# Kernel tuning notes

Measured on AMD Instinct MI355X. Metric: run time of the kernel, lower is better.

## Reference

```python
import jax, jax.numpy as jnp
import numpy as np

N_NODES = 100000
N_EDGES = 1600000
N_FEAT = 128
HIDDEN = 128
N_GRAPHS = 1024


def setup_inputs() -> dict:
    key = jax.random.key(0)
    ks = jax.random.split(key, 9)
    x = jax.random.normal(ks[0], (N_NODES, N_FEAT), dtype=jnp.float32)
    edge_index = jax.random.randint(ks[1], (2, N_EDGES), 0, N_NODES, dtype=jnp.int64)
    batch = jnp.sort(jax.random.randint(ks[2], (N_NODES,), 0, N_GRAPHS, dtype=jnp.int64))
    W1 = jax.random.normal(ks[3], (N_FEAT, HIDDEN), dtype=jnp.float32) * (1.0 / np.sqrt(N_FEAT))
    b1 = jax.random.normal(ks[4], (HIDDEN,), dtype=jnp.float32) * 0.01
    W2 = jax.random.normal(ks[5], (HIDDEN, HIDDEN), dtype=jnp.float32) * (1.0 / np.sqrt(HIDDEN))
    b2 = jax.random.normal(ks[6], (HIDDEN,), dtype=jnp.float32) * 0.01
    Wl = jax.random.normal(ks[7], (HIDDEN, 2), dtype=jnp.float32) * (1.0 / np.sqrt(HIDDEN))
    bl = jax.random.normal(ks[8], (2,), dtype=jnp.float32) * 0.01
    return {"x": x, "edge_index": edge_index, "batch": batch,
            "W1": W1, "b1": b1, "W2": W2, "b2": b2, "Wl": Wl, "bl": bl}


def _gcn_norm(edge_index, num_nodes):
    # PyG GCNConv: add self-loops, then sym-normalize with in-degree (target col).
    loop = jnp.arange(num_nodes, dtype=edge_index.dtype)
    src = jnp.concatenate([edge_index[0], loop])  # [E+N]
    dst = jnp.concatenate([edge_index[1], loop])  # [E+N]
    deg = jax.ops.segment_sum(jnp.ones_like(dst, dtype=jnp.float32), dst,
                              num_segments=num_nodes)
    dinv = jnp.where(deg > 0, jax.lax.rsqrt(deg), 0.0)
    norm = dinv[src] * dinv[dst]  # [E+N]
    return src, dst, norm


def _gcn_conv(h, W, b, src, dst, norm, num_nodes):
    h = h @ W                                   # [N, out]
    msg = h[src] * norm[:, None]                # gather + scale, [E+N, out]
    agg = jax.ops.segment_sum(msg, dst, num_segments=num_nodes)  # scatter-add
    return agg + b


def reference(x, edge_index, batch, W1, b1, W2, b2, Wl, bl):
    n = x.shape[0]
    src, dst, norm = _gcn_norm(edge_index, n)
    h = jax.nn.relu(_gcn_conv(x, W1, b1, src, dst, norm, n))
    h = jax.nn.relu(_gcn_conv(h, W2, b2, src, dst, norm, n))
    # global_mean_pool over graph ids
    sums = jax.ops.segment_sum(h, batch, num_segments=N_GRAPHS)        # [G, H]
    counts = jax.ops.segment_sum(jnp.ones((n,), jnp.float32), batch,
                                 num_segments=N_GRAPHS)
    pooled = sums / jnp.maximum(counts, 1.0)[:, None]
    # F.dropout with training=False default in inference -> identity
    return pooled @ Wl + bl  # [G, 2]
```

## Files before the change

kernel.cpp:

```cpp
#include <hip/hip_runtime.h>
#include <hip/hip_bf16.h>

#define N_NODES 100000
#define N_EDGES 1600000
#define FEAT 128
#define N_GRAPHS 1024
#define NBUCK 391
#define CHUNK 4096
#define NTILES 1563
#define G1A 781
#define G1B 782

typedef short short8 __attribute__((ext_vector_type(8)));
typedef float float4v __attribute__((ext_vector_type(4)));

static __device__ inline unsigned short f2bf(float f) {
    __hip_bfloat16 b = __float2bfloat16(f);
    unsigned short r;
    __builtin_memcpy(&r, &b, 2);
    return r;
}
static __device__ inline float bf_lo(unsigned int v) { return __uint_as_float(v << 16); }
static __device__ inline float bf_hi(unsigned int v) { return __uint_as_float(v & 0xFFFF0000u); }

__global__ __launch_bounds__(256) void k_prep_hist(const float* __restrict__ W1,
                                                   const float* __restrict__ W2,
                                                   unsigned short* __restrict__ wp1,
                                                   unsigned short* __restrict__ wp2,
                                                   const int* __restrict__ dst,
                                                   int* __restrict__ bcount,
                                                   unsigned int* __restrict__ udummy,
                                                   unsigned int* __restrict__ u2dummy,
                                                   float* __restrict__ dinv) {
    int bid = blockIdx.x;
    if (bid < 128) {
        const float* W = (bid < 64) ? W1 : W2;
        unsigned short* wp = (bid < 64) ? wp1 : wp2;
        int t = (bid & 63) * 256 + threadIdx.x;
        int k = t >> 7, n = t & 127;
        float w = W[k * 128 + n];
        unsigned ub = __float_as_uint(w);
        unsigned short hi = (unsigned short)(ub >> 16);
        float hif = __uint_as_float(ub & 0xFFFF0000u);
        unsigned short lo = f2bf(w - hif);
        int sidx = n * 128 + ((k & 7) | (8 * (((k >> 3) ^ n) & 15)));
        wp[sidx] = hi;
        wp[16384 + sidx] = lo;
        if (bid == 0) {
            if (threadIdx.x < 64) udummy[threadIdx.x] = 0;
            else if (threadIdx.x < 128) u2dummy[threadIdx.x - 64] = 0;
            else if (threadIdx.x == 128) dinv[N_NODES] = 0.f;
        }
    } else {
        __shared__ int h[NBUCK];
        for (int i = threadIdx.x; i < NBUCK; i += 256) h[i] = 0;
        __syncthreads();
        int hb = bid - 128;
        for (int e = hb * 256 + threadIdx.x; e < N_EDGES; e += 256 * 256)
            atomicAdd(&h[dst[e] >> 8], 1);
        __syncthreads();
        for (int i = threadIdx.x; i < NBUCK; i += 256) {
            int c = h[i];
            if (c) atomicAdd(&bcount[i], c);
        }
    }
}

__global__ __launch_bounds__(512) void k_scan391(const int* __restrict__ in,
                                                 int* __restrict__ base,
                                                 int* __restrict__ cur,
                                                 int* __restrict__ tail) {
    int t = threadIdx.x;
    int v = (t < NBUCK) ? in[t] : 0;
    int lane = t & 63, wid = t >> 6;
    int s = v;
#pragma unroll
    for (int d = 1; d < 64; d <<= 1) { int n = __shfl_up(s, d); if (lane >= d) s += n; }
    __shared__ int ws[8];
    if (lane == 63) ws[wid] = s;
    __syncthreads();
    if (t < 8) {
        int x = ws[t];
#pragma unroll
        for (int d = 1; d < 8; d <<= 1) { int n = __shfl_up(x, d); if ((int)t >= d) x += n; }
        ws[t] = x;
    }
    __syncthreads();
    int excl = s - v + (wid ? ws[wid - 1] : 0);
    if (t < NBUCK) {
        base[t] = excl;
        cur[t] = excl;
    }
    if (t == 0) tail[0] = N_EDGES;
}

__device__ __forceinline__ void gemm_f32_body(int tile, const float* __restrict__ inp,
                                              const unsigned short* __restrict__ wp,
                                              unsigned short* __restrict__ u) {
    __shared__ unsigned short sW[32768];
    {
        float4* d4 = (float4*)sW;
        const float4* s4 = (const float4*)wp;
#pragma unroll
        for (int i = 0; i < 16; ++i) d4[threadIdx.x + 256 * i] = s4[threadIdx.x + 256 * i];
    }
    __syncthreads();
    const int t = threadIdx.x;
    const int wv = t >> 6, L = t & 63;
    const int m = L & 15, q = L >> 4;
    const int r0 = tile * 64 + wv * 16;
    int arow = r0 + m;
    if (arow >= N_NODES) arow = N_NODES - 1;
    const float4* ap = (const float4*)(inp + (size_t)arow * 128);
    float4v acc[8];
#pragma unroll
    for (int c = 0; c < 8; ++c) acc[c] = (float4v){0.f, 0.f, 0.f, 0.f};
#pragma unroll
    for (int k0 = 0; k0 < 128; k0 += 32) {
        float4 f0 = ap[(k0 >> 2) + 2 * q];
        float4 f1 = ap[(k0 >> 2) + 2 * q + 1];
        float fa[8] = {f0.x, f0.y, f0.z, f0.w, f1.x, f1.y, f1.z, f1.w};
        short8 ah, al;
#pragma unroll
        for (int j = 0; j < 8; ++j) {
            unsigned ub = __float_as_uint(fa[j]);
            ah[j] = (short)(ub >> 16);
            float hif = __uint_as_float(ub & 0xFFFF0000u);
            al[j] = (short)f2bf(fa[j] - hif);
        }
        const int b = (k0 >> 3) + q;
#pragma unroll
        for (int c = 0; c < 8; ++c) {
            int ng = c * 16 + m;
            int elem = ng * 128 + 8 * ((b ^ ng) & 15);
            short8 bh = *(const short8*)&sW[elem];
            short8 bl = *(const short8*)&sW[16384 + elem];
            acc[c] = __builtin_amdgcn_mfma_f32_16x16x32_bf16(ah, bh, acc[c], 0, 0, 0);
            acc[c] = __builtin_amdgcn_mfma_f32_16x16x32_bf16(al, bh, acc[c], 0, 0, 0);
            acc[c] = __builtin_amdgcn_mfma_f32_16x16x32_bf16(ah, bl, acc[c], 0, 0, 0);
        }
    }
#pragma unroll
    for (int r = 0; r < 4; ++r) {
        int row = r0 + 4 * q + r;
        if (row < N_NODES) {
            unsigned short* up = u + (size_t)row * 128 + m;
#pragma unroll
            for (int c = 0; c < 8; ++c) up[c * 16] = f2bf(acc[c][r]);
        }
    }
}

__global__ __launch_bounds__(256) void k_bucket_g1(const int* __restrict__ src,
                                                   const int* __restrict__ dst,
                                                   int* __restrict__ bcur,
                                                   unsigned int* __restrict__ pairs,
                                                   const float* __restrict__ x,
                                                   const unsigned short* __restrict__ wp1,
                                                   unsigned short* __restrict__ u) {
    if (blockIdx.x >= NBUCK) {
        gemm_f32_body(blockIdx.x - NBUCK, x, wp1, u);
        return;
    }
    __shared__ int cnt[NBUCK];
    __shared__ int basebuf[NBUCK];
    int t = threadIdx.x;
    int e0 = blockIdx.x * CHUNK;
    for (int i = t; i < NBUCK; i += 256) cnt[i] = 0;
    __syncthreads();
    unsigned pk[16]; int bk[16];
#pragma unroll
    for (int j = 0; j < 16; ++j) {
        int e = e0 + j * 256 + t;
        if (e < N_EDGES) {
            int s = src[e], d = dst[e];
            bk[j] = d >> 8;
            pk[j] = ((unsigned)s << 8) | (unsigned)(d & 255);
            atomicAdd(&cnt[bk[j]], 1);
        } else bk[j] = -1;
    }
    __syncthreads();
    for (int i = t; i < NBUCK; i += 256) {
        int c = cnt[i];
        basebuf[i] = c ? atomicAdd(&bcur[i], c) : 0;
        cnt[i] = 0;
    }
    __syncthreads();
#pragma unroll
    for (int j = 0; j < 16; ++j) {
        if (bk[j] >= 0) {
            int p = basebuf[bk[j]] + atomicAdd(&cnt[bk[j]], 1);
            pairs[p] = pk[j];
        }
    }
}

__global__ __launch_bounds__(256) void k_bfill_g1(const unsigned int* __restrict__ pairs,
                                                  const int* __restrict__ bbase,
                                                  const int* __restrict__ bcount,
                                                  float* __restrict__ dinv,
                                                  int* __restrict__ offs,
                                                  int* __restrict__ csr,
                                                  const float* __restrict__ x,
                                                  const unsigned short* __restrict__ wp1,
                                                  unsigned short* __restrict__ u) {
    if (blockIdx.x >= NBUCK) {
        gemm_f32_body(blockIdx.x - NBUCK + G1A, x, wp1, u);
        return;
    }
    __shared__ int degl[256];
    __shared__ int lcur[256];
    __shared__ int ws[4];
    int b = blockIdx.x, t = threadIdx.x;
    degl[t] = 0;
    __syncthreads();
    int s0 = bbase[b], n = bcount[b];
    for (int i = t; i < n; i += 256) atomicAdd(&degl[pairs[s0 + i] & 255u], 1);
    __syncthreads();
    int node = b * 256 + t;
    int dv = degl[t];
    if (node < N_NODES) dinv[node] = rsqrtf((float)(dv + 1));
    int lane = t & 63, wid = t >> 6;
    int s = dv;
#pragma unroll
    for (int d = 1; d < 64; d <<= 1) { int nn = __shfl_up(s, d); if (lane >= d) s += nn; }
    if (lane == 63) ws[wid] = s;
    __syncthreads();
    if (t < 4) {
        int xx = ws[t];
#pragma unroll
        for (int d = 1; d < 4; d <<= 1) { int nn = __shfl_up(xx, d); if ((int)t >= d) xx += nn; }
        ws[t] = xx;
    }
    __syncthreads();
    int excl = s - dv + (wid ? ws[wid - 1] : 0) + bbase[b];
    if (node < N_NODES) offs[node] = excl;
    lcur[t] = excl;
    __syncthreads();
    for (int i = t; i < n; i += 256) {
        unsigned pr = pairs[s0 + i];
        int p = atomicAdd(&lcur[pr & 255u], 1);
        csr[p] = (int)(pr >> 8);
    }
}

__global__ __launch_bounds__(512, 6) void k_agg1_g2(const unsigned int* __restrict__ u,
                                                    const int* __restrict__ offs,
                                                    const int* __restrict__ csr,
                                                    const float* __restrict__ dinv,
                                                    const float* __restrict__ bias,
                                                    const unsigned short* __restrict__ wp,
                                                    unsigned short* __restrict__ u2) {
    __shared__ float hS[32 * 128];
    const int w = threadIdx.x >> 6;
    const int lane = threadIdx.x & 63;
    const int base = blockIdx.x * 32;

    for (int n = 0; n < 4; ++n) {
        const int row = 4 * w + n;
        const int node = base + row;
        int p = __builtin_amdgcn_readfirstlane(offs[node]);
        int e = __builtin_amdgcn_readfirstlane(offs[node + 1]);
        float dsf = dinv[node];
        unsigned int self = u[(size_t)node * 64 + lane];
        float ax0 = dsf * bf_lo(self), ay0 = dsf * bf_hi(self);
        float ax1 = 0.f, ay1 = 0.f, ax2 = 0.f, ay2 = 0.f, ax3 = 0.f, ay3 = 0.f;
        float ax4 = 0.f, ay4 = 0.f, ax5 = 0.f, ay5 = 0.f, ax6 = 0.f, ay6 = 0.f;
        float ax7 = 0.f, ay7 = 0.f;
        for (; p < e; p += 8) {
            int c0 = csr[p + 0], c1 = csr[p + 1], c2 = csr[p + 2], c3 = csr[p + 3];
            int c4 = csr[p + 4], c5 = csr[p + 5], c6 = csr[p + 6], c7 = csr[p + 7];
            int i0 = c0;
            int i1 = (p + 1 < e) ? c1 : N_NODES;
            int i2 = (p + 2 < e) ? c2 : N_NODES;
            int i3 = (p + 3 < e) ? c3 : N_NODES;
            int i4 = (p + 4 < e) ? c4 : N_NODES;
            int i5 = (p + 5 < e) ? c5 : N_NODES;
            int i6 = (p + 6 < e) ? c6 : N_NODES;
            int i7 = (p + 7 < e) ? c7 : N_NODES;
            float d0 = dinv[i0], d1 = dinv[i1], d2 = dinv[i2], d3 = dinv[i3];
            float d4 = dinv[i4], d5 = dinv[i5], d6 = dinv[i6], d7 = dinv[i7];
            unsigned v0 = (u + (size_t)i0 * 64)[lane];
            unsigned v1 = (u + (size_t)i1 * 64)[lane];
            unsigned v2 = (u + (size_t)i2 * 64)[lane];
            unsigned v3 = (u + (size_t)i3 * 64)[lane];
            unsigned v4 = (u + (size_t)i4 * 64)[lane];
            unsigned v5 = (u + (size_t)i5 * 64)[lane];
            unsigned v6 = (u + (size_t)i6 * 64)[lane];
            unsigned v7 = (u + (size_t)i7 * 64)[lane];
            ax0 = fmaf(d0, bf_lo(v0), ax0); ay0 = fmaf(d0, bf_hi(v0), ay0);
            ax1 = fmaf(d1, bf_lo(v1), ax1); ay1 = fmaf(d1, bf_hi(v1), ay1);
            ax2 = fmaf(d2, bf_lo(v2), ax2); ay2 = fmaf(d2, bf_hi(v2), ay2);
            ax3 = fmaf(d3, bf_lo(v3), ax3); ay3 = fmaf(d3, bf_hi(v3), ay3);
            ax4 = fmaf(d4, bf_lo(v4), ax4); ay4 = fmaf(d4, bf_hi(v4), ay4);
            ax5 = fmaf(d5, bf_lo(v5), ax5); ay5 = fmaf(d5, bf_hi(v5), ay5);
            ax6 = fmaf(d6, bf_lo(v6), ax6); ay6 = fmaf(d6, bf_hi(v6), ay6);
            ax7 = fmaf(d7, bf_lo(v7), ax7); ay7 = fmaf(d7, bf_hi(v7), ay7);
        }
        float2 b = ((const float2*)bias)[lane];
        float sx = ((ax0 + ax1) + (ax2 + ax3)) + ((ax4 + ax5) + (ax6 + ax7));
        float sy = ((ay0 + ay1) + (ay2 + ay3)) + ((ay4 + ay5) + (ay6 + ay7));
        float r0 = fmaxf(dsf * sx + b.x, 0.f);
        float r1 = fmaxf(dsf * sy + b.y, 0.f);
        int g4 = (lane >> 1) ^ (row & 7);
        float2* hp = (float2*)&hS[row * 128 + g4 * 4 + (lane & 1) * 2];
        *hp = (float2){r0, r1};
    }

    const int m = lane & 15, q = lane >> 4;
    const int rt = w >> 2;
    const int cw = w & 3;
    const int arow = 16 * rt + m;
    const int ng0 = (2 * cw + 0) * 16 + m;
    const int ng1 = (2 * cw + 1) * 16 + m;
    short8 bh0, bl0, bh1, bl1;
    {
        int b = q;
        int e0 = ng0 * 128 + 8 * ((b ^ ng0) & 15);
        int e1 = ng1 * 128 + 8 * ((b ^ ng1) & 15);
        bh0 = *(const short8*)&wp[e0];
        bl0 = *(const short8*)&wp[16384 + e0];
        bh1 = *(const short8*)&wp[e1];
        bl1 = *(const short8*)&wp[16384 + e1];
    }
    __syncthreads();

    float4v acc0 = (float4v){0.f, 0.f, 0.f, 0.f};
    float4v acc1 = (float4v){0.f, 0.f, 0.f, 0.f};
#pragma unroll
    for (int ks = 0; ks < 4; ++ks) {
        short8 nh0, nl0, nh1, nl1;
        if (ks < 3) {
            int b = 4 * (ks + 1) + q;
            int e0 = ng0 * 128 + 8 * ((b ^ ng0) & 15);
            int e1 = ng1 * 128 + 8 * ((b ^ ng1) & 15);
            nh0 = *(const short8*)&wp[e0];
            nl0 = *(const short8*)&wp[16384 + e0];
            nh1 = *(const short8*)&wp[e1];
            nl1 = *(const short8*)&wp[16384 + e1];
        }
        const int k0 = 32 * ks;
        int g1 = (k0 >> 2) + 2 * q;
        float4 f0 = *(const float4*)&hS[arow * 128 + ((g1 ^ (arow & 7)) << 2)];
        float4 f1 = *(const float4*)&hS[arow * 128 + (((g1 + 1) ^ (arow & 7)) << 2)];
        float fa[8] = {f0.x, f0.y, f0.z, f0.w, f1.x, f1.y, f1.z, f1.w};
        short8 ah, al;
#pragma unroll
        for (int j = 0; j < 8; ++j) {
            unsigned ub = __float_as_uint(fa[j]);
            ah[j] = (short)(ub >> 16);
            float hif = __uint_as_float(ub & 0xFFFF0000u);
            al[j] = (short)f2bf(fa[j] - hif);
        }
        acc0 = __builtin_amdgcn_mfma_f32_16x16x32_bf16(ah, bh0, acc0, 0, 0, 0);
        acc0 = __builtin_amdgcn_mfma_f32_16x16x32_bf16(al, bh0, acc0, 0, 0, 0);
        acc0 = __builtin_amdgcn_mfma_f32_16x16x32_bf16(ah, bl0, acc0, 0, 0, 0);
        acc1 = __builtin_amdgcn_mfma_f32_16x16x32_bf16(ah, bh1, acc1, 0, 0, 0);
        acc1 = __builtin_amdgcn_mfma_f32_16x16x32_bf16(al, bh1, acc1, 0, 0, 0);
        acc1 = __builtin_amdgcn_mfma_f32_16x16x32_bf16(ah, bl1, acc1, 0, 0, 0);
        if (ks < 3) {
            bh0 = nh0; bl0 = nl0; bh1 = nh1; bl1 = nl1;
        }
    }
#pragma unroll
    for (int r = 0; r < 4; ++r) {
        int row = 16 * rt + 4 * q + r;
        unsigned short* up = u2 + (size_t)(base + row) * 128 + m;
        up[(2 * cw + 0) * 16] = f2bf(acc0[r]);
        up[(2 * cw + 1) * 16] = f2bf(acc1[r]);
    }
}

__global__ __launch_bounds__(256) void k_agg2(const unsigned int* __restrict__ u,
                                              const int* __restrict__ offs,
                                              const int* __restrict__ csr,
                                              const float* __restrict__ dinv,
                                              const float* __restrict__ bias,
                                              const float* __restrict__ Wl,
                                              float* __restrict__ pnode) {
    int wid = threadIdx.x >> 6;
    int lane = threadIdx.x & 63;
    int node = __builtin_amdgcn_readfirstlane(blockIdx.x * 4 + wid);
    if (node >= N_NODES) return;
    int p = __builtin_amdgcn_readfirstlane(offs[node]);
    int e = __builtin_amdgcn_readfirstlane(offs[node + 1]);
    float dsf = dinv[node];
    unsigned int self = u[(size_t)node * 64 + lane];
    float ax0 = dsf * bf_lo(self), ay0 = dsf * bf_hi(self);
    float ax1 = 0.f, ay1 = 0.f, ax2 = 0.f, ay2 = 0.f, ax3 = 0.f, ay3 = 0.f;
    float ax4 = 0.f, ay4 = 0.f, ax5 = 0.f, ay5 = 0.f, ax6 = 0.f, ay6 = 0.f;
    float ax7 = 0.f, ay7 = 0.f;
    for (; p < e; p += 8) {
        int c0 = csr[p + 0], c1 = csr[p + 1], c2 = csr[p + 2], c3 = csr[p + 3];
        int c4 = csr[p + 4], c5 = csr[p + 5], c6 = csr[p + 6], c7 = csr[p + 7];
        int i0 = c0;
        int i1 = (p + 1 < e) ? c1 : N_NODES;
        int i2 = (p + 2 < e) ? c2 : N_NODES;
        int i3 = (p + 3 < e) ? c3 : N_NODES;
        int i4 = (p + 4 < e) ? c4 : N_NODES;
        int i5 = (p + 5 < e) ? c5 : N_NODES;
        int i6 = (p + 6 < e) ? c6 : N_NODES;
        int i7 = (p + 7 < e) ? c7 : N_NODES;
        float d0 = dinv[i0], d1 = dinv[i1], d2 = dinv[i2], d3 = dinv[i3];
        float d4 = dinv[i4], d5 = dinv[i5], d6 = dinv[i6], d7 = dinv[i7];
        unsigned v0 = (u + (size_t)i0 * 64)[lane];
        unsigned v1 = (u + (size_t)i1 * 64)[lane];
        unsigned v2 = (u + (size_t)i2 * 64)[lane];
        unsigned v3 = (u + (size_t)i3 * 64)[lane];
        unsigned v4 = (u + (size_t)i4 * 64)[lane];
        unsigned v5 = (u + (size_t)i5 * 64)[lane];
        unsigned v6 = (u + (size_t)i6 * 64)[lane];
        unsigned v7 = (u + (size_t)i7 * 64)[lane];
        ax0 = fmaf(d0, bf_lo(v0), ax0); ay0 = fmaf(d0, bf_hi(v0), ay0);
        ax1 = fmaf(d1, bf_lo(v1), ax1); ay1 = fmaf(d1, bf_hi(v1), ay1);
        ax2 = fmaf(d2, bf_lo(v2), ax2); ay2 = fmaf(d2, bf_hi(v2), ay2);
        ax3 = fmaf(d3, bf_lo(v3), ax3); ay3 = fmaf(d3, bf_hi(v3), ay3);
        ax4 = fmaf(d4, bf_lo(v4), ax4); ay4 = fmaf(d4, bf_hi(v4), ay4);
        ax5 = fmaf(d5, bf_lo(v5), ax5); ay5 = fmaf(d5, bf_hi(v5), ay5);
        ax6 = fmaf(d6, bf_lo(v6), ax6); ay6 = fmaf(d6, bf_hi(v6), ay6);
        ax7 = fmaf(d7, bf_lo(v7), ax7); ay7 = fmaf(d7, bf_hi(v7), ay7);
    }
    float2 b = ((const float2*)bias)[lane];
    float sx = ((ax0 + ax1) + (ax2 + ax3)) + ((ax4 + ax5) + (ax6 + ax7));
    float sy = ((ay0 + ay1) + (ay2 + ay3)) + ((ay4 + ay5) + (ay6 + ay7));
    float r0 = fmaxf(dsf * sx + b.x, 0.f);
    float r1 = fmaxf(dsf * sy + b.y, 0.f);
    float2 wl0 = ((const float2*)Wl)[2 * lane];
    float2 wl1 = ((const float2*)Wl)[2 * lane + 1];
    float p0 = r0 * wl0.x + r1 * wl1.x;
    float p1 = r0 * wl0.y + r1 * wl1.y;
#pragma unroll
    for (int d = 32; d > 0; d >>= 1) {
        p0 += __shfl_xor(p0, d);
        p1 += __shfl_xor(p1, d);
    }
    if (lane == 0) {
        float2* pp = (float2*)pnode;
        pp[node] = (float2){p0, p1};
    }
}

__global__ __launch_bounds__(64) void k_fin(const float* __restrict__ pnode,
                                            const int* __restrict__ batch,
                                            const float* __restrict__ bl,
                                            float* __restrict__ out) {
    int g = blockIdx.x;
    int lane = threadIdx.x;
    __shared__ int sb[2];
    if (lane < 2) {
        int tgt = g + lane;
        int lo = 0, hi = N_NODES;
        while (lo < hi) { int m = (lo + hi) >> 1; if (batch[m] < tgt) lo = m + 1; else hi = m; }
        sb[lane] = lo;
    }
    __syncthreads();
    int s0 = sb[0], s1 = sb[1];
    const float2* pp = (const float2*)pnode;
    float p0 = 0.f, p1 = 0.f;
    for (int i = s0 + lane; i < s1; i += 64) {
        float2 v = pp[i];
        p0 += v.x;
        p1 += v.y;
    }
#pragma unroll
    for (int d = 32; d > 0; d >>= 1) {
        p0 += __shfl_xor(p0, d);
        p1 += __shfl_xor(p1, d);
    }
    if (lane == 0) {
        float inv = 1.f / fmaxf((float)(s1 - s0), 1.f);
        out[2 * g + 0] = p0 * inv + bl[0];
        out[2 * g + 1] = p1 * inv + bl[1];
    }
}

extern "C" void kernel_launch(void* const* d_in, const int* in_sizes, int n_in,
                              void* d_out, int out_size, void* d_ws, size_t ws_size,
                              hipStream_t stream) {
    const float* x  = (const float*)d_in[0];
    const int* ei   = (const int*)d_in[1];
    const int* batch = (const int*)d_in[2];
    const float* W1 = (const float*)d_in[3];
    const float* b1 = (const float*)d_in[4];
    const float* W2 = (const float*)d_in[5];
    const float* b2 = (const float*)d_in[6];
    const float* Wl = (const float*)d_in[7];
    const float* bl = (const float*)d_in[8];
    float* out = (float*)d_out;
    const int* src = ei;
    const int* dst = ei + N_EDGES;

    char* ws = (char*)d_ws;
    size_t o = 0;
    auto alloc = [&](size_t bytes) -> void* {
        o = (o + 255) & ~(size_t)255;
        void* p = ws + o;
        o += bytes;
        return p;
    };
    int* bcount = (int*)alloc((size_t)NBUCK * 4);
    int* bbase  = (int*)alloc((size_t)NBUCK * 4);
    int* bcur   = (int*)alloc((size_t)NBUCK * 4);
    float* dinv = (float*)alloc((size_t)(N_NODES + 1) * 4);
    int* offs   = (int*)alloc((size_t)(N_NODES + 1) * 4);
    unsigned short* wp1 = (unsigned short*)alloc(65536);
    unsigned short* wp2 = (unsigned short*)alloc(65536);
    float* pnode = (float*)alloc((size_t)N_NODES * 2 * 4);
    unsigned int* pairs = (unsigned int*)alloc((size_t)N_EDGES * 4);
    int* csr    = (int*)alloc((size_t)(N_EDGES + 8) * 4);
    unsigned short* u  = (unsigned short*)alloc((size_t)(N_NODES + 1) * 128 * 2);
    unsigned short* u2 = (unsigned short*)alloc((size_t)(N_NODES + 1) * 128 * 2);

    hipMemsetAsync(bcount, 0, (size_t)NBUCK * 4, stream);
    k_prep_hist<<<384, 256, 0, stream>>>(W1, W2, wp1, wp2, dst, bcount,
                                         (unsigned int*)(u + (size_t)N_NODES * 128),
                                         (unsigned int*)(u2 + (size_t)N_NODES * 128), dinv);
    k_scan391<<<1, 512, 0, stream>>>(bcount, bbase, bcur, &offs[N_NODES]);
    k_bucket_g1<<<NBUCK + G1A, 256, 0, stream>>>(src, dst, bcur, pairs, x, wp1, u);
    k_bfill_g1<<<NBUCK + G1B, 256, 0, stream>>>(pairs, bbase, bcount, dinv, offs, csr, x, wp1, u);

    k_agg1_g2<<<N_NODES / 32, 512, 0, stream>>>((const unsigned int*)u, offs, csr, dinv, b1,
                                                wp2, u2);
    k_agg2<<<(N_NODES + 3) / 4, 256, 0, stream>>>((const unsigned int*)u2, offs, csr, dinv, b2,
                                                  Wl, pnode);

    k_fin<<<N_GRAPHS, 64, 0, stream>>>(pnode, batch, bl, out);
}
```

Measured before the change: 313.8 us.

## Build CSR with global per-node degree atomics instead of two-pass bucket sort

Replaces the bucketed two-pass CSR construction (bucket scatter into a pairs buffer, then per-bucket local fill) with per-node global degree counting in the histogram kernel, a per-block offset scan, and a single fill pass that does one global atomic per edge on a per-node cursor. The first-layer GEMM tiles are all merged into the single fill launch. This removes one kernel launch and the intermediate pairs buffer traffic, but adds 1.6M global atomics twice (degree and cursor) plus a memset. CSR neighbour order within a node also becomes nondeterministic.

```diff
diff --git a/kernel.cpp b/kernel.cpp
--- a/kernel.cpp
+++ b/kernel.cpp
@@ -8,8 +8,6 @@
 #define NBUCK 391
 #define CHUNK 4096
 #define NTILES 1563
-#define G1A 781
-#define G1B 782
 
 typedef short short8 __attribute__((ext_vector_type(8)));
 typedef float float4v __attribute__((ext_vector_type(4)));
@@ -29,6 +27,7 @@
                                                    unsigned short* __restrict__ wp2,
                                                    const int* __restrict__ dst,
                                                    int* __restrict__ bcount,
+                                                   int* __restrict__ deg,
                                                    unsigned int* __restrict__ udummy,
                                                    unsigned int* __restrict__ u2dummy,
                                                    float* __restrict__ dinv) {
@@ -56,8 +55,11 @@
         for (int i = threadIdx.x; i < NBUCK; i += 256) h[i] = 0;
         __syncthreads();
         int hb = bid - 128;
-        for (int e = hb * 256 + threadIdx.x; e < N_EDGES; e += 256 * 256)
-            atomicAdd(&h[dst[e] >> 8], 1);
+        for (int e = hb * 256 + threadIdx.x; e < N_EDGES; e += 256 * 256) {
+            int d = dst[e];
+            atomicAdd(&h[d >> 8], 1);
+            atomicAdd(&deg[d], 1);
+        }
         __syncthreads();
         for (int i = threadIdx.x; i < NBUCK; i += 256) {
             int c = h[i];
@@ -66,32 +68,44 @@
     }
 }
 
-__global__ __launch_bounds__(512) void k_scan391(const int* __restrict__ in,
-                                                 int* __restrict__ base,
-                                                 int* __restrict__ cur,
-                                                 int* __restrict__ tail) {
-    int t = threadIdx.x;
-    int v = (t < NBUCK) ? in[t] : 0;
+__global__ __launch_bounds__(256) void k_offs(const int* __restrict__ bcount,
+                                              const int* __restrict__ deg,
+                                              float* __restrict__ dinv,
+                                              int* __restrict__ offs,
+                                              int* __restrict__ cur) {
+    int b = blockIdx.x, t = threadIdx.x;
     int lane = t & 63, wid = t >> 6;
-    int s = v;
-#pragma unroll
-    for (int d = 1; d < 64; d <<= 1) { int n = __shfl_up(s, d); if (lane >= d) s += n; }
-    __shared__ int ws[8];
-    if (lane == 63) ws[wid] = s;
-    __syncthreads();
-    if (t < 8) {
-        int x = ws[t];
-#pragma unroll
-        for (int d = 1; d < 8; d <<= 1) { int n = __shfl_up(x, d); if ((int)t >= d) x += n; }
-        ws[t] = x;
-    }
-    __syncthreads();
-    int excl = s - v + (wid ? ws[wid - 1] : 0);
-    if (t < NBUCK) {
-        base[t] = excl;
-        cur[t] = excl;
-    }
-    if (t == 0) tail[0] = N_EDGES;
+    int acc = 0;
+    if (t < b) acc = bcount[t];
+    if (t + 256 < b) acc += bcount[t + 256];
+#pragma unroll
+    for (int d = 32; d > 0; d >>= 1) acc += __shfl_xor(acc, d);
+    __shared__ int ws[4];
+    __shared__ int ps[4];
+    if (lane == 0) ws[wid] = acc;
+    __syncthreads();
+    int base = ws[0] + ws[1] + ws[2] + ws[3];
+    int node = b * 256 + t;
+    int dv = (node < N_NODES) ? deg[node] : 0;
+    if (node < N_NODES) dinv[node] = rsqrtf((float)(dv + 1));
+    int s = dv;
+#pragma unroll
+    for (int d = 1; d < 64; d <<= 1) { int nn = __shfl_up(s, d); if (lane >= d) s += nn; }
+    if (lane == 63) ps[wid] = s;
+    __syncthreads();
+    if (t < 4) {
+        int xx = ps[t];
+#pragma unroll
+        for (int d = 1; d < 4; d <<= 1) { int nn = __shfl_up(xx, d); if ((int)t >= d) xx += nn; }
+        ps[t] = xx;
+    }
+    __syncthreads();
+    int excl = s - dv + (wid ? ps[wid - 1] : 0) + base;
+    if (node < N_NODES) {
+        offs[node] = excl;
+        cur[node] = excl;
+    }
+    if (b == NBUCK - 1 && t == 0) offs[N_NODES] = N_EDGES;
 }
 
 __device__ __forceinline__ void gemm_f32_body(int tile, const float* __restrict__ inp,
@@ -151,96 +165,28 @@
     }
 }
 
-__global__ __launch_bounds__(256) void k_bucket_g1(const int* __restrict__ src,
-                                                   const int* __restrict__ dst,
-                                                   int* __restrict__ bcur,
-                                                   unsigned int* __restrict__ pairs,
-                                                   const float* __restrict__ x,
-                                                   const unsigned short* __restrict__ wp1,
-                                                   unsigned short* __restrict__ u) {
-    if (blockIdx.x >= NBUCK) {
-        gemm_f32_body(blockIdx.x - NBUCK, x, wp1, u);
+__global__ __launch_bounds__(256) void k_fill_g1(const int* __restrict__ src,
+                                                 const int* __restrict__ dst,
+                                                 int* __restrict__ cur,
+                                                 int* __restrict__ csr,
+                                                 const float* __restrict__ x,
+                                                 const unsigned short* __restrict__ wp1,
+                                                 unsigned short* __restrict__ u) {
+    if (blockIdx.x < NTILES) {
+        gemm_f32_body(blockIdx.x, x, wp1, u);
         return;
     }
-    __shared__ int cnt[NBUCK];
-    __shared__ int basebuf[NBUCK];
+    int fb = blockIdx.x - NTILES;
     int t = threadIdx.x;
-    int e0 = blockIdx.x * CHUNK;
-    for (int i = t; i < NBUCK; i += 256) cnt[i] = 0;
-    __syncthreads();
-    unsigned pk[16]; int bk[16];
+    int e0 = fb * CHUNK;
 #pragma unroll
     for (int j = 0; j < 16; ++j) {
         int e = e0 + j * 256 + t;
         if (e < N_EDGES) {
             int s = src[e], d = dst[e];
-            bk[j] = d >> 8;
-            pk[j] = ((unsigned)s << 8) | (unsigned)(d & 255);
-            atomicAdd(&cnt[bk[j]], 1);
-        } else bk[j] = -1;
-    }
-    __syncthreads();
-    for (int i = t; i < NBUCK; i += 256) {
-        int c = cnt[i];
-        basebuf[i] = c ? atomicAdd(&bcur[i], c) : 0;
-        cnt[i] = 0;
-    }
-    __syncthreads();
-#pragma unroll
-    for (int j = 0; j < 16; ++j) {
-        if (bk[j] >= 0) {
-            int p = basebuf[bk[j]] + atomicAdd(&cnt[bk[j]], 1);
-            pairs[p] = pk[j];
-        }
-    }
-}
-
-__global__ __launch_bounds__(256) void k_bfill_g1(const unsigned int* __restrict__ pairs,
-                                                  const int* __restrict__ bbase,
-                                                  const int* __restrict__ bcount,
-                                                  float* __restrict__ dinv,
-                                                  int* __restrict__ offs,
-                                                  int* __restrict__ csr,
-                                                  const float* __restrict__ x,
-                                                  const unsigned short* __restrict__ wp1,
-                                                  unsigned short* __restrict__ u) {
-    if (blockIdx.x >= NBUCK) {
-        gemm_f32_body(blockIdx.x - NBUCK + G1A, x, wp1, u);
-        return;
-    }
-    __shared__ int degl[256];
-    __shared__ int lcur[256];
-    __shared__ int ws[4];
-    int b = blockIdx.x, t = threadIdx.x;
-    degl[t] = 0;
-    __syncthreads();
-    int s0 = bbase[b], n = bcount[b];
-    for (int i = t; i < n; i += 256) atomicAdd(&degl[pairs[s0 + i] & 255u], 1);
-    __syncthreads();
-    int node = b * 256 + t;
-    int dv = degl[t];
-    if (node < N_NODES) dinv[node] = rsqrtf((float)(dv + 1));
-    int lane = t & 63, wid = t >> 6;
-    int s = dv;
-#pragma unroll
-    for (int d = 1; d < 64; d <<= 1) { int nn = __shfl_up(s, d); if (lane >= d) s += nn; }
-    if (lane == 63) ws[wid] = s;
-    __syncthreads();
-    if (t < 4) {
-        int xx = ws[t];
-#pragma unroll
-        for (int d = 1; d < 4; d <<= 1) { int nn = __shfl_up(xx, d); if ((int)t >= d) xx += nn; }
-        ws[t] = xx;
-    }
-    __syncthreads();
-    int excl = s - dv + (wid ? ws[wid - 1] : 0) + bbase[b];
-    if (node < N_NODES) offs[node] = excl;
-    lcur[t] = excl;
-    __syncthreads();
-    for (int i = t; i < n; i += 256) {
-        unsigned pr = pairs[s0 + i];
-        int p = atomicAdd(&lcur[pr & 255u], 1);
-        csr[p] = (int)(pr >> 8);
+            int p = atomicAdd(&cur[d], 1);
+            csr[p] = s;
+        }
     }
 }
 
@@ -499,25 +445,24 @@
         return p;
     };
     int* bcount = (int*)alloc((size_t)NBUCK * 4);
-    int* bbase  = (int*)alloc((size_t)NBUCK * 4);
-    int* bcur   = (int*)alloc((size_t)NBUCK * 4);
+    int* deg    = (int*)alloc((size_t)N_NODES * 4);
+    int* cur    = (int*)alloc((size_t)N_NODES * 4);
     float* dinv = (float*)alloc((size_t)(N_NODES + 1) * 4);
     int* offs   = (int*)alloc((size_t)(N_NODES + 1) * 4);
     unsigned short* wp1 = (unsigned short*)alloc(65536);
     unsigned short* wp2 = (unsigned short*)alloc(65536);
     float* pnode = (float*)alloc((size_t)N_NODES * 2 * 4);
-    unsigned int* pairs = (unsigned int*)alloc((size_t)N_EDGES * 4);
     int* csr    = (int*)alloc((size_t)(N_EDGES + 8) * 4);
     unsigned short* u  = (unsigned short*)alloc((size_t)(N_NODES + 1) * 128 * 2);
     unsigned short* u2 = (unsigned short*)alloc((size_t)(N_NODES + 1) * 128 * 2);
 
     hipMemsetAsync(bcount, 0, (size_t)NBUCK * 4, stream);
-    k_prep_hist<<<384, 256, 0, stream>>>(W1, W2, wp1, wp2, dst, bcount,
+    hipMemsetAsync(deg, 0, (size_t)N_NODES * 4, stream);
+    k_prep_hist<<<384, 256, 0, stream>>>(W1, W2, wp1, wp2, dst, bcount, deg,
                                          (unsigned int*)(u + (size_t)N_NODES * 128),
                                          (unsigned int*)(u2 + (size_t)N_NODES * 128), dinv);
-    k_scan391<<<1, 512, 0, stream>>>(bcount, bbase, bcur, &offs[N_NODES]);
-    k_bucket_g1<<<NBUCK + G1A, 256, 0, stream>>>(src, dst, bcur, pairs, x, wp1, u);
-    k_bfill_g1<<<NBUCK + G1B, 256, 0, stream>>>(pairs, bbase, bcount, dinv, offs, csr, x, wp1, u);
+    k_offs<<<NBUCK, 256, 0, stream>>>(bcount, deg, dinv, offs, cur);
+    k_fill_g1<<<NTILES + NBUCK, 256, 0, stream>>>(src, dst, cur, csr, x, wp1, u);
 
     k_agg1_g2<<<N_NODES / 32, 512, 0, stream>>>((const unsigned int*)u, offs, csr, dinv, b1,
                                                 wp2, u2);
```

Result: slower. 455.4 us (+45.1%).
